# Kernel tuning notes

Hardware: AMD Instinct MI355X
Metric: run time of the kernel (lower is better)

The kernel has to match this reference:

```python
import jax, jax.numpy as jnp
import numpy as np

T = 36  # num_frames


def box_cxcywh_to_xyxy(b):
    cx, cy, w, h = jnp.split(b, 4, axis=-1)
    return jnp.concatenate([cx - 0.5 * w, cy - 0.5 * h, cx + 0.5 * w, cy + 0.5 * h], axis=-1)


def multi_iou(b1, b2):
    # b1: [Q,1,T,4], b2: [1,N,T,4], xyxy -> iou [Q,N,T]
    lt = jnp.maximum(b1[..., :2], b2[..., :2])
    rb = jnp.minimum(b1[..., 2:], b2[..., 2:])
    wh = jnp.clip(rb - lt, 0.0)
    inter = wh[..., 0] * wh[..., 1]
    a1 = (b1[..., 2] - b1[..., 0]) * (b1[..., 3] - b1[..., 1])
    a2 = (b2[..., 2] - b2[..., 0]) * (b2[..., 3] - b2[..., 1])
    union = a1 + a2 - inter
    return inter / union


def setup_inputs() -> dict:
    key = jax.random.key(0)
    k1, k2, k3, k4, k5, k6 = jax.random.split(key, 6)
    Q, N, C = 2048, 128, 42
    return {
        "pred_logits": jax.random.normal(k1, (T * Q, C), dtype=jnp.float32),
        "pred_boxes": jax.random.uniform(k2, (T * Q, 4), dtype=jnp.float32),
        "tgt_labels": jax.random.randint(k3, (N * T,), 0, C - 1),
        "tgt_boxes": jax.random.uniform(k4, (N * T, 4), dtype=jnp.float32),
        "tgt_valid": jax.random.randint(k5, (N * T,), 0, 2, dtype=jnp.int32),
        "tgt_original_valid": jax.random.randint(k6, (N * T,), 0, 2, dtype=jnp.int32),
    }


def reference(pred_logits, pred_boxes, tgt_labels, tgt_boxes, tgt_valid, tgt_original_valid):
    # Cost-matrix computation of SoftMaxHungarianMatcher (cost_class=cost_bbox=cost_giou=1,
    # use_giou=False, use_l1_distance_sum=False). The scipy linear_sum_assignment step is
    # CPU-serial / non-tensor and excluded; output is the [Q,N] cost fed to it.
    C = pred_logits.shape[-1]
    Q = pred_logits.shape[0] // T
    N = tgt_labels.shape[0] // T
    num_classes = C - 1  # background index

    probs = jax.nn.softmax(pred_logits, axis=-1).reshape(T, Q, C).transpose(1, 0, 2)  # [Q,T,C]
    boxes = pred_boxes.reshape(T, Q, 4).transpose(1, 0, 2)                            # [Q,T,4]
    tboxes = tgt_boxes.reshape(N, T, 4)
    valid = tgt_valid.reshape(N, T).astype(probs.dtype)                               # [N,T]
    ovalid = tgt_original_valid.reshape(N, T)
    ids = jnp.where(ovalid == 0, num_classes, tgt_labels.reshape(N, T))               # [N,T]

    denom = valid.sum(-1)  # [N] (per-instance count of valid frames)

    # class cost: -mean_t p(q, t, ids[n,t]) over valid frames
    gathered = probs[:, jnp.arange(T)[None, :], ids]                                  # [Q,N,T]
    class_cost = -(gathered * valid).sum(-1) / denom                                  # [Q,N]

    # bbox L1 cost: mean over (valid frames, 4 coords)
    l1 = jnp.abs(boxes[:, None] - tboxes[None]).mean(-1)                              # [Q,N,T]
    bbox_cost = (l1 * valid).sum(-1) / denom                                          # [Q,N]

    # IoU cost: -mean_t iou over valid frames
    iou = multi_iou(box_cxcywh_to_xyxy(boxes)[:, None], box_cxcywh_to_xyxy(tboxes)[None])
    iou_cost = -(iou * valid).sum(-1) / denom                                         # [Q,N]

    return class_cost + bbox_cost + iou_cost
```

## Files before the change

### kernel.cpp

```cpp
#include <hip/hip_runtime.h>
#include <hip/hip_bf16.h>


constexpr int T = 36;
constexpr int Q = 2048;
constexpr int C = 42;
constexpr int N = 128;

__global__ __launch_bounds__(256) void softmax_transpose_kernel(
    const float* __restrict__ logits, float* __restrict__ P2) {
  constexpr int QB = 64;
  constexpr int LDS_STRIDE = C + 1;
  const int t = blockIdx.y;
  const int q0 = blockIdx.x * QB;
  const int tid = threadIdx.x;

  __shared__ float tile[QB * LDS_STRIDE];
  __shared__ float rmax[QB];
  __shared__ float rinv[QB];

  const float* src = logits + ((size_t)t * Q + q0) * C;
  for (int i = tid; i < QB * C; i += 256) {
    int r = i / C, c = i % C;
    tile[r * LDS_STRIDE + c] = src[i];
  }
  __syncthreads();

  if (tid < QB) {
    const float* row = tile + tid * LDS_STRIDE;
    float m = -1e30f;
    for (int c = 0; c < C; ++c) m = fmaxf(m, row[c]);
    float s = 0.f;
    for (int c = 0; c < C; ++c) s += __expf(row[c] - m);
    rmax[tid] = m;
    rinv[tid] = 1.f / s;
  }
  __syncthreads();

  for (int i = tid; i < QB * C; i += 256) {
    int c = i >> 6;
    int r = i & 63;
    float v = __expf(tile[r * LDS_STRIDE + c] - rmax[r]) * rinv[r];
    P2[(size_t)(t * C + c) * Q + q0 + r] = v;
  }
}

__global__ __launch_bounds__(256) void cost_kernel(
    const float* __restrict__ P2, const float* __restrict__ pred_boxes,
    const int* __restrict__ labels, const float* __restrict__ tboxes,
    const int* __restrict__ valid, const int* __restrict__ ovalid,
    float* __restrict__ out) {
  constexpr int QB = 64;
  constexpr int NB = 16;
  constexpr int RES_STRIDE = NB + 1;

  const int q0 = blockIdx.x * QB;
  const int n0 = blockIdx.y * NB;
  const int tid = threadIdx.x;
  const int lane = tid & 63;
  const int sub = tid >> 6;
  const int q = q0 + lane;

  __shared__ float s_tb[NB * T * 4];
  __shared__ float s_val[NB * T];
  __shared__ int s_id[NB * T];
  __shared__ float s_res[QB * RES_STRIDE];

  for (int i = tid; i < NB * T; i += 256) {
    int n = n0 + i / T;
    int t = i % T;
    int g = n * T + t;
    s_val[i] = (float)valid[g];
    s_id[i] = (ovalid[g] == 0) ? (C - 1) : labels[g];
    float4 tb = ((const float4*)tboxes)[g];
    s_tb[i * 4 + 0] = tb.x;
    s_tb[i * 4 + 1] = tb.y;
    s_tb[i * 4 + 2] = tb.z;
    s_tb[i * 4 + 3] = tb.w;
  }
  __syncthreads();

  float acc[4] = {0.f, 0.f, 0.f, 0.f};
  float vsum[4] = {0.f, 0.f, 0.f, 0.f};

  for (int t = 0; t < T; ++t) {
    float4 pb = ((const float4*)pred_boxes)[t * Q + q];
    float px1 = pb.x - 0.5f * pb.z, py1 = pb.y - 0.5f * pb.w;
    float px2 = pb.x + 0.5f * pb.z, py2 = pb.y + 0.5f * pb.w;
    float pa = pb.z * pb.w;
    const float* probs_t = P2 + (size_t)t * C * Q + q;

#pragma unroll
    for (int j = 0; j < 4; ++j) {
      int nl = sub * 4 + j;
      int idx = nl * T + t;
      float v = s_val[idx];
      int id = s_id[idx];
      float p = probs_t[(size_t)id * Q];
      float tcx = s_tb[idx * 4 + 0], tcy = s_tb[idx * 4 + 1];
      float tw = s_tb[idx * 4 + 2], th = s_tb[idx * 4 + 3];
      float l1 = 0.25f * (fabsf(pb.x - tcx) + fabsf(pb.y - tcy) +
                          fabsf(pb.z - tw) + fabsf(pb.w - th));
      float tx1 = tcx - 0.5f * tw, ty1 = tcy - 0.5f * th;
      float tx2 = tcx + 0.5f * tw, ty2 = tcy + 0.5f * th;
      float iw = fminf(px2, tx2) - fmaxf(px1, tx1);
      float ih = fminf(py2, ty2) - fmaxf(py1, ty1);
      iw = fmaxf(iw, 0.f);
      ih = fmaxf(ih, 0.f);
      float inter = iw * ih;
      float uni = pa + tw * th - inter;
      float iou = inter / uni;
      acc[j] += v * (l1 - p - iou);
      vsum[j] += v;
    }
  }

#pragma unroll
  for (int j = 0; j < 4; ++j) {
    int nl = sub * 4 + j;
    s_res[lane * RES_STRIDE + nl] = acc[j] / vsum[j];
  }
  __syncthreads();

  int r = tid >> 2;
  int c4 = tid & 3;
  float4 o;
  o.x = s_res[r * RES_STRIDE + c4 * 4 + 0];
  o.y = s_res[r * RES_STRIDE + c4 * 4 + 1];
  o.z = s_res[r * RES_STRIDE + c4 * 4 + 2];
  o.w = s_res[r * RES_STRIDE + c4 * 4 + 3];
  ((float4*)(out + (size_t)(q0 + r) * N + n0))[c4] = o;
}

extern "C" void kernel_launch(void* const* d_in, const int* in_sizes, int n_in,
                              void* d_out, int out_size, void* d_ws, size_t ws_size,
                              hipStream_t stream) {
  const float* logits = (const float*)d_in[0];
  const float* pboxes = (const float*)d_in[1];
  const int* labels = (const int*)d_in[2];
  const float* tboxes = (const float*)d_in[3];
  const int* valid = (const int*)d_in[4];
  const int* ovalid = (const int*)d_in[5];
  float* out = (float*)d_out;

  float* P2 = (float*)d_ws;

  dim3 g1(Q / 64, T);
  softmax_transpose_kernel<<<g1, 256, 0, stream>>>(logits, P2);

  dim3 g2(Q / 64, N / 16);
  cost_kernel<<<g2, 256, 0, stream>>>(P2, pboxes, labels, tboxes, valid, ovalid, out);
}
```

Measured before the change: 99.20 us.

## Skip invalid frames and assign one target per wavefront in cost kernel

The cost kernel now gives each wavefront a single target instead of four and builds a grid four times larger along N. Valid flag and class id are packed into one int in LDS, and the box math and probability gather are skipped for invalid frames through a branch that is uniform across the wavefront. The reciprocal of the valid-frame count is computed once per target. This cuts wasted ALU and gather work and raises parallelism, at the cost of redundant pred_boxes loads across more blocks, with only a quarter of threads storing output.

```diff
diff --git a/kernel.cpp b/kernel.cpp
--- a/kernel.cpp
+++ b/kernel.cpp
@@ -50,86 +50,72 @@
     const int* __restrict__ labels, const float* __restrict__ tboxes,
     const int* __restrict__ valid, const int* __restrict__ ovalid,
     float* __restrict__ out) {
-  constexpr int QB = 64;
-  constexpr int NB = 16;
+  constexpr int NB = 4;
   constexpr int RES_STRIDE = NB + 1;
 
-  const int q0 = blockIdx.x * QB;
+  const int q0 = blockIdx.x * 64;
   const int n0 = blockIdx.y * NB;
   const int tid = threadIdx.x;
   const int lane = tid & 63;
   const int sub = tid >> 6;
   const int q = q0 + lane;
 
-  __shared__ float s_tb[NB * T * 4];
-  __shared__ float s_val[NB * T];
-  __shared__ int s_id[NB * T];
-  __shared__ float s_res[QB * RES_STRIDE];
+  __shared__ float4 s_tb[NB * T];
+  __shared__ int s_idv[NB * T];
+  __shared__ float s_rden[NB];
+  __shared__ float s_res[64 * RES_STRIDE];
 
   for (int i = tid; i < NB * T; i += 256) {
     int n = n0 + i / T;
     int t = i % T;
     int g = n * T + t;
-    s_val[i] = (float)valid[g];
-    s_id[i] = (ovalid[g] == 0) ? (C - 1) : labels[g];
-    float4 tb = ((const float4*)tboxes)[g];
-    s_tb[i * 4 + 0] = tb.x;
-    s_tb[i * 4 + 1] = tb.y;
-    s_tb[i * 4 + 2] = tb.z;
-    s_tb[i * 4 + 3] = tb.w;
+    s_idv[i] = ((ovalid[g] == 0) ? (C - 1) : labels[g]) | (valid[g] << 8);
+    s_tb[i] = ((const float4*)tboxes)[g];
+  }
+  if (tid < NB) {
+    int n = n0 + tid;
+    int s = 0;
+    for (int t = 0; t < T; ++t) s += valid[n * T + t];
+    s_rden[tid] = 1.f / (float)s;
   }
   __syncthreads();
 
-  float acc[4] = {0.f, 0.f, 0.f, 0.f};
-  float vsum[4] = {0.f, 0.f, 0.f, 0.f};
+  float acc = 0.f;
+  const float* probs_base = P2 + q;
 
   for (int t = 0; t < T; ++t) {
-    float4 pb = ((const float4*)pred_boxes)[t * Q + q];
-    float px1 = pb.x - 0.5f * pb.z, py1 = pb.y - 0.5f * pb.w;
-    float px2 = pb.x + 0.5f * pb.z, py2 = pb.y + 0.5f * pb.w;
-    float pa = pb.z * pb.w;
-    const float* probs_t = P2 + (size_t)t * C * Q + q;
+    int pk = s_idv[sub * T + t];
+    if (pk & 0x100) {
+      float4 pb = ((const float4*)pred_boxes)[t * Q + q];
+      float4 tb = s_tb[sub * T + t];
+      int id = pk & 0xff;
+      float p = probs_base[(size_t)(t * C + id) * Q];
 
-#pragma unroll
-    for (int j = 0; j < 4; ++j) {
-      int nl = sub * 4 + j;
-      int idx = nl * T + t;
-      float v = s_val[idx];
-      int id = s_id[idx];
-      float p = probs_t[(size_t)id * Q];
-      float tcx = s_tb[idx * 4 + 0], tcy = s_tb[idx * 4 + 1];
-      float tw = s_tb[idx * 4 + 2], th = s_tb[idx * 4 + 3];
-      float l1 = 0.25f * (fabsf(pb.x - tcx) + fabsf(pb.y - tcy) +
-                          fabsf(pb.z - tw) + fabsf(pb.w - th));
-      float tx1 = tcx - 0.5f * tw, ty1 = tcy - 0.5f * th;
-      float tx2 = tcx + 0.5f * tw, ty2 = tcy + 0.5f * th;
-      float iw = fminf(px2, tx2) - fmaxf(px1, tx1);
-      float ih = fminf(py2, ty2) - fmaxf(py1, ty1);
-      iw = fmaxf(iw, 0.f);
-      ih = fmaxf(ih, 0.f);
+      float l1 = 0.25f * (fabsf(pb.x - tb.x) + fabsf(pb.y - tb.y) +
+                          fabsf(pb.z - tb.z) + fabsf(pb.w - tb.w));
+      float px1 = pb.x - 0.5f * pb.z, py1 = pb.y - 0.5f * pb.w;
+      float px2 = pb.x + 0.5f * pb.z, py2 = pb.y + 0.5f * pb.w;
+      float tx1 = tb.x - 0.5f * tb.z, ty1 = tb.y - 0.5f * tb.w;
+      float tx2 = tb.x + 0.5f * tb.z, ty2 = tb.y + 0.5f * tb.w;
+      float iw = fmaxf(fminf(px2, tx2) - fmaxf(px1, tx1), 0.f);
+      float ih = fmaxf(fminf(py2, ty2) - fmaxf(py1, ty1), 0.f);
       float inter = iw * ih;
-      float uni = pa + tw * th - inter;
-      float iou = inter / uni;
-      acc[j] += v * (l1 - p - iou);
-      vsum[j] += v;
+      float uni = pb.z * pb.w + tb.z * tb.w - inter;
+      acc += l1 - p - inter / uni;
     }
   }
 
-#pragma unroll
-  for (int j = 0; j < 4; ++j) {
-    int nl = sub * 4 + j;
-    s_res[lane * RES_STRIDE + nl] = acc[j] / vsum[j];
-  }
+  s_res[lane * RES_STRIDE + sub] = acc * s_rden[sub];
   __syncthreads();
 
-  int r = tid >> 2;
-  int c4 = tid & 3;
-  float4 o;
-  o.x = s_res[r * RES_STRIDE + c4 * 4 + 0];
-  o.y = s_res[r * RES_STRIDE + c4 * 4 + 1];
-  o.z = s_res[r * RES_STRIDE + c4 * 4 + 2];
-  o.w = s_res[r * RES_STRIDE + c4 * 4 + 3];
-  ((float4*)(out + (size_t)(q0 + r) * N + n0))[c4] = o;
+  if (tid < 64) {
+    float4 o;
+    o.x = s_res[tid * RES_STRIDE + 0];
+    o.y = s_res[tid * RES_STRIDE + 1];
+    o.z = s_res[tid * RES_STRIDE + 2];
+    o.w = s_res[tid * RES_STRIDE + 3];
+    *(float4*)(out + (size_t)(q0 + tid) * N + n0) = o;
+  }
 }
 
 extern "C" void kernel_launch(void* const* d_in, const int* in_sizes, int n_in,
@@ -148,6 +134,6 @@
   dim3 g1(Q / 64, T);
   softmax_transpose_kernel<<<g1, 256, 0, stream>>>(logits, P2);
 
-  dim3 g2(Q / 64, N / 16);
+  dim3 g2(Q / 64, N / 4);
   cost_kernel<<<g2, 256, 0, stream>>>(P2, pboxes, labels, tboxes, valid, ovalid, out);
 }
```

After: 88.11 us. 1.13x faster.
